# Performance work log

Measured on AMD Instinct MI355X. Metric: run time of the kernel, lower is better.

## Reference

```python
import jax, jax.numpy as jnp
import numpy as np

B = 65536
D_IN = 8
H1, H2 = 256, 256


def setup_inputs() -> dict:
    key = jax.random.key(0)
    ks = jax.random.split(key, 12)
    def lin(kw, kb, fan_in, fan_out):
        s = 1.0 / np.sqrt(fan_in)
        W = jax.random.uniform(kw, (fan_out, fan_in), jnp.float32, -s, s)
        b = jax.random.uniform(kb, (fan_out,), jnp.float32, -s, s)
        return W, b
    W0, b0 = lin(ks[0], ks[1], D_IN, H1)
    W1, b1 = lin(ks[2], ks[3], H1, H2)
    W2, b2 = lin(ks[4], ks[5], H2, 1)
    W3, b3 = lin(ks[6], ks[7], 1, 8)
    x_batch = jax.random.normal(ks[8], (B, D_IN), jnp.float32)
    scores_x_batch = jax.random.normal(ks[9], (B, D_IN), jnp.float32)
    c = jnp.zeros((), jnp.float32)  # init_val parameter
    return {"x_batch": x_batch, "scores_x_batch": scores_x_batch,
            "W0": W0, "b0": b0, "W1": W1, "b1": b1,
            "W2": W2, "b2": b2, "W3": W3, "b3": b3, "c": c}


def reference(x_batch, scores_x_batch, W0, b0, W1, b1, W2, b2, W3, b3, c):
    # singleforwardpass: tanh on all layers except the last
    def single(x):  # x: [8] -> [8]
        y = jnp.tanh(W0 @ x + b0)
        y = jnp.tanh(W1 @ y + b1)
        y = jnp.tanh(W2 @ y + b2)
        return W3 @ y + b3

    eye = jnp.eye(D_IN, dtype=x_batch.dtype)

    def per_sample(x, score):
        # jacobian(single, x).diag().sum() + dot(single(x), score) + c
        u, lin_fn = jax.linearize(single, x)
        J = jax.vmap(lin_fn)(eye)        # [8, 8] (columns of Jacobian as rows)
        div = jnp.trace(J)               # sum of Jacobian diagonal
        return c + div + jnp.dot(u, score)

    return jax.vmap(per_sample)(x_batch, scores_x_batch)  # [B]
```

## Files before the change

kernel.cpp:

```cpp
#include <hip/hip_runtime.h>
#include <hip/hip_bf16.h>

#define B_TOTAL 65536
#define H 256
#define TS 64
#define THREADS 512
#define STRIDE 264
#define KK 2.8853900817779268f

#define WS_W1   0
#define WS_W0B  65536
#define WS_AUX  67584
#define WS_XB   73728
#define WS_NEED_BYTES (147456 + 1048576)

typedef __attribute__((ext_vector_type(8))) short bf16x8;
typedef __attribute__((ext_vector_type(4))) float f32x4;

__device__ __forceinline__ float rsig(float kz) {
    float e = __builtin_amdgcn_exp2f(kz);
    return __builtin_amdgcn_rcpf(e + 1.0f);
}
__device__ __forceinline__ void tanh_r(float x, float& t, float& r) {
    r = rsig(KK * x);
    t = fmaf(-2.0f, r, 1.0f);
}
__device__ __forceinline__ float bf2f(ushort b) {
    union { unsigned u; float f; } v; v.u = ((unsigned)b) << 16;
    return v.f;
}
__device__ __forceinline__ ushort f2bf(float f) {
    union { float f; unsigned u; } v; v.f = f;
    unsigned r = v.u + 0x7fffu + ((v.u >> 16) & 1u);
    return (ushort)(r >> 16);
}
__device__ __forceinline__ ushort2 cvt2(float a, float b) {
    union { __hip_bfloat162 h; ushort2 u; } v;
    v.h = __float22bfloat162_rn(make_float2(a, b));
    return v.u;
}
__device__ __forceinline__ bf16x8 pack8(float4 a, float4 b) {
    union { bf16x8 v; ushort2 u[4]; } r;
    r.u[0] = cvt2(a.x, a.y); r.u[1] = cvt2(a.z, a.w);
    r.u[2] = cvt2(b.x, b.y); r.u[3] = cvt2(b.z, b.w);
    return r.v;
}

__global__ void prep(const float* __restrict__ W1, const float* __restrict__ W0,
                     const float* __restrict__ W3, const float* __restrict__ b0,
                     const float* __restrict__ b1, const float* __restrict__ W2,
                     const float* __restrict__ x, ushort* __restrict__ ws) {
    const int blk = blockIdx.x, tid = threadIdx.x;
    if (blk < 32) {
        int g = blk * 256 + tid;
        int jt = g >> 9;
        int ks = (g >> 6) & 7;
        int l  = g & 63;
        int row = jt * 16 + (l & 15);
        int k0  = ks * 32 + (l >> 4) * 8;
        ushort* dst = ws + WS_W1 + (size_t)g * 8;
        const float* src = W1 + (size_t)row * H + k0;
#pragma unroll
        for (int t = 0; t < 8; ++t) dst[t] = f2bf(src[t]);
    } else if (blk == 32) {
        const int j = tid;
        const float* wr = W0 + (size_t)j * 8;
        float4 wa = *(const float4*)wr, wb = *(const float4*)(wr + 4);
        float4 w3a = *(const float4*)W3, w3b = *(const float4*)(W3 + 4);
        float g0 = wa.x * w3a.x + wa.y * w3a.y + wa.z * w3a.z + wa.w * w3a.w
                 + wb.x * w3b.x + wb.y * w3b.y + wb.z * w3b.z + wb.w * w3b.w;
        float* aux = (float*)(ws + WS_AUX);
        aux[j]        = 4.f * g0;
        aux[256 + j]  = KK * b0[j];
        aux[512 + j]  = KK * b1[j];
        aux[768 + j]  = -2.f * W2[j];
        aux[1024 + j] = 4.f * W2[j];
        *(bf16x8*)(ws + WS_W0B + (size_t)j * 8) = pack8(wa, wb);
    } else {
        const int s = (blk - 33) * 256 + tid;
        const float* xr = x + (size_t)s * 8;
        *(bf16x8*)(ws + WS_XB + (size_t)s * 8) =
            pack8(*(const float4*)xr, *(const float4*)(xr + 4));
    }
}

template<int XB>
__launch_bounds__(THREADS, 4)
__global__ void fused_mlp(const float* __restrict__ x_batch,
                          const float* __restrict__ scores,
                          const float* __restrict__ b2,
                          const float* __restrict__ W3, const float* __restrict__ b3,
                          const float* __restrict__ cptr,
                          const ushort* __restrict__ ws,
                          float* __restrict__ out) {
    __shared__ ushort Y0[TS][STRIDE];
    __shared__ ushort DG[TS][STRIDE];
    __shared__ float  Z2p[8][TS];
    __shared__ float  Trp[8][TS];

    const int tid  = threadIdx.x;
    const int lane = tid & 63;
    const int w    = tid >> 6;
    const int bs   = blockIdx.x * TS;
    const int cl   = lane & 15;
    const int q    = lane >> 4;
    const int rq   = q * 4;
    const int j0   = w * 32;

    const ushort* pW  = ws + WS_W1 + (size_t)(2 * w) * 4096 + (size_t)lane * 8;
    const ushort* w0b = ws + WS_W0B;
    const float*  aux = (const float*)(ws + WS_AUX);
    const float*  G4  = aux;
    const float*  KB0 = aux + 256;
    const float*  KB1 = aux + 512;
    const float*  WN  = aux + 768;
    const float*  W4  = aux + 1024;
    const ushort* xb  = ws + WS_XB;

    f32x4 l0[2][4];
    {
        bf16x8 bx[4];
#pragma unroll
        for (int st = 0; st < 4; ++st) {
            bf16x8 p = (bf16x8){0, 0, 0, 0, 0, 0, 0, 0};
            if (q == 0) {
                if (XB) {
                    p = *(const bf16x8*)(xb + (size_t)(bs + st * 16 + cl) * 8);
                } else {
                    const float* xr = x_batch + (size_t)(bs + st * 16 + cl) * 8;
                    p = pack8(*(const float4*)xr, *(const float4*)(xr + 4));
                }
            }
            bx[st] = p;
        }
        bf16x8 af0 = *(const bf16x8*)(w0b + (size_t)(j0 + cl) * 8);
        bf16x8 af1 = *(const bf16x8*)(w0b + (size_t)(j0 + 16 + cl) * 8);
#pragma unroll
        for (int st = 0; st < 4; ++st) {
            f32x4 z = (f32x4){0.f, 0.f, 0.f, 0.f};
            l0[0][st] = __builtin_amdgcn_mfma_f32_16x16x32_bf16(af0, bx[st], z, 0, 0, 0);
            l0[1][st] = __builtin_amdgcn_mfma_f32_16x16x32_bf16(af1, bx[st], z, 0, 0, 0);
        }
    }

    {
        float4 kb0 = *(const float4*)(KB0 + j0 + rq);
        float4 kb1 = *(const float4*)(KB0 + j0 + 16 + rq);
        float4 g40 = *(const float4*)(G4 + j0 + rq);
        float4 g41 = *(const float4*)(G4 + j0 + 16 + rq);
#pragma unroll
        for (int st = 0; st < 4; ++st) {
            const int row = st * 16 + cl;
#pragma unroll
            for (int jt = 0; jt < 2; ++jt) {
                f32x4 z = l0[jt][st];
                float4 kb = jt ? kb1 : kb0;
                float4 g4 = jt ? g41 : g40;
                float r0 = rsig(fmaf(KK, z[0], kb.x));
                float r1 = rsig(fmaf(KK, z[1], kb.y));
                float r2 = rsig(fmaf(KK, z[2], kb.z));
                float r3 = rsig(fmaf(KK, z[3], kb.w));
                float t0 = fmaf(-2.f, r0, 1.f), t1 = fmaf(-2.f, r1, 1.f);
                float t2 = fmaf(-2.f, r2, 1.f), t3 = fmaf(-2.f, r3, 1.f);
                ushort2 lo = cvt2(t0, t1), hi = cvt2(t2, t3);
                ushort4 vv; vv.x = lo.x; vv.y = lo.y; vv.z = hi.x; vv.w = hi.y;
                *(ushort4*)&Y0[row][j0 + jt * 16 + rq] = vv;
                float m0 = r0 * g4.x, m1 = r1 * g4.y, m2 = r2 * g4.z, m3 = r3 * g4.w;
                float d0 = fmaf(-m0, r0, m0), d1 = fmaf(-m1, r1, m1);
                float d2 = fmaf(-m2, r2, m2), d3 = fmaf(-m3, r3, m3);
                lo = cvt2(d0, d1); hi = cvt2(d2, d3);
                vv.x = lo.x; vv.y = lo.y; vv.z = hi.x; vv.w = hi.y;
                *(ushort4*)&DG[row][j0 + jt * 16 + rq] = vv;
            }
        }
    }
    __syncthreads();

    f32x4 facc[2][4], bacc[2][4];
#pragma unroll
    for (int jt = 0; jt < 2; ++jt)
#pragma unroll
        for (int st = 0; st < 4; ++st) {
            facc[jt][st] = (f32x4){0.f, 0.f, 0.f, 0.f};
            bacc[jt][st] = (f32x4){0.f, 0.f, 0.f, 0.f};
        }
#pragma unroll
    for (int ks = 0; ks < 8; ++ks) {
        const int k0 = ks * 32 + q * 8;
        bf16x8 wf0 = *(const bf16x8*)(pW + (size_t)ks * 512);
        bf16x8 wf1 = *(const bf16x8*)(pW + 4096 + (size_t)ks * 512);
#pragma unroll
        for (int st = 0; st < 4; ++st) {
            bf16x8 by = *(const bf16x8*)&Y0[st * 16 + cl][k0];
            bf16x8 bd = *(const bf16x8*)&DG[st * 16 + cl][k0];
            facc[0][st] = __builtin_amdgcn_mfma_f32_16x16x32_bf16(wf0, by, facc[0][st], 0, 0, 0);
            facc[1][st] = __builtin_amdgcn_mfma_f32_16x16x32_bf16(wf1, by, facc[1][st], 0, 0, 0);
            bacc[0][st] = __builtin_amdgcn_mfma_f32_16x16x32_bf16(wf0, bd, bacc[0][st], 0, 0, 0);
            bacc[1][st] = __builtin_amdgcn_mfma_f32_16x16x32_bf16(wf1, bd, bacc[1][st], 0, 0, 0);
        }
    }

    {
        float4 kb0 = *(const float4*)(KB1 + j0 + rq);
        float4 kb1 = *(const float4*)(KB1 + j0 + 16 + rq);
        float4 wn0 = *(const float4*)(WN + j0 + rq);
        float4 wn1 = *(const float4*)(WN + j0 + 16 + rq);
        float4 w40 = *(const float4*)(W4 + j0 + rq);
        float4 w41 = *(const float4*)(W4 + j0 + 16 + rq);
        float zp0 = 0.25f * ((w40.x + w40.y) + (w40.z + w40.w)
                           + (w41.x + w41.y) + (w41.z + w41.w));
#pragma unroll
        for (int st = 0; st < 4; ++st) {
            float zp = zp0, tp = 0.f;
#pragma unroll
            for (int jt = 0; jt < 2; ++jt) {
                f32x4 z  = facc[jt][st];
                f32x4 mm = bacc[jt][st];
                float4 kb = jt ? kb1 : kb0;
                float4 wn = jt ? wn1 : wn0;
                float4 w4 = jt ? w41 : w40;
                float r0 = rsig(fmaf(KK, z[0], kb.x));
                float r1 = rsig(fmaf(KK, z[1], kb.y));
                float r2 = rsig(fmaf(KK, z[2], kb.z));
                float r3 = rsig(fmaf(KK, z[3], kb.w));
                zp = fmaf(wn.x, r0, zp); zp = fmaf(wn.y, r1, zp);
                zp = fmaf(wn.z, r2, zp); zp = fmaf(wn.w, r3, zp);
                float m0 = r0 * w4.x, m1 = r1 * w4.y, m2 = r2 * w4.z, m3 = r3 * w4.w;
                float a0 = fmaf(-m0, r0, m0), a1 = fmaf(-m1, r1, m1);
                float a2 = fmaf(-m2, r2, m2), a3 = fmaf(-m3, r3, m3);
                tp = fmaf(a0, mm[0], tp); tp = fmaf(a1, mm[1], tp);
                tp = fmaf(a2, mm[2], tp); tp = fmaf(a3, mm[3], tp);
            }
            zp += __shfl_xor(zp, 16);
            zp += __shfl_xor(zp, 32);
            tp += __shfl_xor(tp, 16);
            tp += __shfl_xor(tp, 32);
            if (lane < 16) {
                Z2p[w][st * 16 + lane] = zp;
                Trp[w][st * 16 + lane] = tp;
            }
        }
    }
    __syncthreads();

    if (tid < TS) {
        const int s = tid;
        float z2 = b2[0], tr = 0.f;
#pragma unroll
        for (int k = 0; k < 8; ++k) { z2 += Z2p[k][s]; tr += Trp[k][s]; }
        float y2, r2;
        tanh_r(z2, y2, r2);
        float m2 = 4.0f * r2;
        float dy2 = fmaf(-m2, r2, m2);
        float4 w3a = *(const float4*)W3;
        float4 w3b = *(const float4*)(W3 + 4);
        float4 b3a = *(const float4*)b3;
        float4 b3b = *(const float4*)(b3 + 4);
        const float* sc = scores + (size_t)(bs + s) * 8;
        float4 s0 = *(const float4*)sc;
        float4 s1 = *(const float4*)(sc + 4);
        float p1 = w3a.x * s0.x + w3a.y * s0.y + w3a.z * s0.z + w3a.w * s0.w
                 + w3b.x * s1.x + w3b.y * s1.y + w3b.z * s1.z + w3b.w * s1.w;
        float p2 = b3a.x * s0.x + b3a.y * s0.y + b3a.z * s0.z + b3a.w * s0.w
                 + b3b.x * s1.x + b3b.y * s1.y + b3b.z * s1.z + b3b.w * s1.w;
        out[bs + s] = cptr[0] + dy2 * tr + fmaf(y2, p1, p2);
    }
}

extern "C" void kernel_launch(void* const* d_in, const int* in_sizes, int n_in,
                              void* d_out, int out_size, void* d_ws, size_t ws_size,
                              hipStream_t stream) {
    const float* x  = (const float*)d_in[0];
    const float* sc = (const float*)d_in[1];
    const float* W0 = (const float*)d_in[2];
    const float* b0 = (const float*)d_in[3];
    const float* W1 = (const float*)d_in[4];
    const float* b1 = (const float*)d_in[5];
    const float* W2 = (const float*)d_in[6];
    const float* b2 = (const float*)d_in[7];
    const float* W3 = (const float*)d_in[8];
    const float* b3 = (const float*)d_in[9];
    const float* c  = (const float*)d_in[10];
    float* out = (float*)d_out;
    ushort* ws = (ushort*)d_ws;

    const bool xb = ws_size >= (size_t)WS_NEED_BYTES;
    hipLaunchKernelGGL(prep, dim3(xb ? 289 : 33), dim3(256), 0, stream,
                       W1, W0, W3, b0, b1, W2, x, ws);
    if (xb) {
        hipLaunchKernelGGL(fused_mlp<1>, dim3(B_TOTAL / TS), dim3(THREADS), 0, stream,
                           x, sc, b2, W3, b3, c, ws, out);
    } else {
        hipLaunchKernelGGL(fused_mlp<0>, dim3(B_TOTAL / TS), dim3(THREADS), 0, stream,
                           x, sc, b2, W3, b3, c, ws, out);
    }
}
```

Measured before the change: 30.92 us.

## Process two sample tiles per block, hoisting constants and prefetching next tile's inputs

Each block now loops over two 64-sample tiles instead of one, halving the grid size. Per-neuron constants (biases, gains, layer-2 weights) are loaded once per block and reused across both tiles. The next tile's x inputs are prefetched during the current tile's layer-1 MFMA work. Costs are fewer blocks to spread across CUs (512 instead of 1024), an extra barrier per tile and higher register pressure.

```diff
diff --git a/kernel.cpp b/kernel.cpp
--- a/kernel.cpp
+++ b/kernel.cpp
@@ -4,6 +4,7 @@
 #define B_TOTAL 65536
 #define H 256
 #define TS 64
+#define NT 2
 #define THREADS 512
 #define STRIDE 264
 #define KK 2.8853900817779268f
@@ -95,13 +96,13 @@
                           float* __restrict__ out) {
     __shared__ ushort Y0[TS][STRIDE];
     __shared__ ushort DG[TS][STRIDE];
-    __shared__ float  Z2p[8][TS];
-    __shared__ float  Trp[8][TS];
+    __shared__ float  Z2p[8][NT][TS];
+    __shared__ float  Trp[8][NT][TS];
 
     const int tid  = threadIdx.x;
     const int lane = tid & 63;
     const int w    = tid >> 6;
-    const int bs   = blockIdx.x * TS;
+    const int bs0  = blockIdx.x * (TS * NT);
     const int cl   = lane & 15;
     const int q    = lane >> 4;
     const int rq   = q * 4;
@@ -117,44 +118,57 @@
     const float*  W4  = aux + 1024;
     const ushort* xb  = ws + WS_XB;
 
-    f32x4 l0[2][4];
-    {
-        bf16x8 bx[4];
-#pragma unroll
-        for (int st = 0; st < 4; ++st) {
-            bf16x8 p = (bf16x8){0, 0, 0, 0, 0, 0, 0, 0};
-            if (q == 0) {
-                if (XB) {
-                    p = *(const bf16x8*)(xb + (size_t)(bs + st * 16 + cl) * 8);
-                } else {
-                    const float* xr = x_batch + (size_t)(bs + st * 16 + cl) * 8;
-                    p = pack8(*(const float4*)xr, *(const float4*)(xr + 4));
-                }
-            }
-            bx[st] = p;
-        }
-        bf16x8 af0 = *(const bf16x8*)(w0b + (size_t)(j0 + cl) * 8);
-        bf16x8 af1 = *(const bf16x8*)(w0b + (size_t)(j0 + 16 + cl) * 8);
-#pragma unroll
-        for (int st = 0; st < 4; ++st) {
-            f32x4 z = (f32x4){0.f, 0.f, 0.f, 0.f};
-            l0[0][st] = __builtin_amdgcn_mfma_f32_16x16x32_bf16(af0, bx[st], z, 0, 0, 0);
-            l0[1][st] = __builtin_amdgcn_mfma_f32_16x16x32_bf16(af1, bx[st], z, 0, 0, 0);
-        }
-    }
-
-    {
-        float4 kb0 = *(const float4*)(KB0 + j0 + rq);
-        float4 kb1 = *(const float4*)(KB0 + j0 + 16 + rq);
-        float4 g40 = *(const float4*)(G4 + j0 + rq);
-        float4 g41 = *(const float4*)(G4 + j0 + 16 + rq);
+    float4 kb00 = *(const float4*)(KB0 + j0 + rq);
+    float4 kb01 = *(const float4*)(KB0 + j0 + 16 + rq);
+    float4 g40  = *(const float4*)(G4 + j0 + rq);
+    float4 g41  = *(const float4*)(G4 + j0 + 16 + rq);
+    float4 kb10 = *(const float4*)(KB1 + j0 + rq);
+    float4 kb11 = *(const float4*)(KB1 + j0 + 16 + rq);
+    float4 wn0  = *(const float4*)(WN + j0 + rq);
+    float4 wn1  = *(const float4*)(WN + j0 + 16 + rq);
+    float4 w40  = *(const float4*)(W4 + j0 + rq);
+    float4 w41  = *(const float4*)(W4 + j0 + 16 + rq);
+    float zp0 = 0.25f * ((w40.x + w40.y) + (w40.z + w40.w)
+                       + (w41.x + w41.y) + (w41.z + w41.w));
+
+    bf16x8 bx[4];
+#pragma unroll
+    for (int st = 0; st < 4; ++st) {
+        bf16x8 p = (bf16x8){0, 0, 0, 0, 0, 0, 0, 0};
+        if (q == 0) {
+            if (XB) {
+                p = *(const bf16x8*)(xb + (size_t)(bs0 + st * 16 + cl) * 8);
+            } else {
+                const float* xr = x_batch + (size_t)(bs0 + st * 16 + cl) * 8;
+                p = pack8(*(const float4*)xr, *(const float4*)(xr + 4));
+            }
+        }
+        bx[st] = p;
+    }
+
+#pragma unroll
+    for (int t = 0; t < NT; ++t) {
+        const int bs = bs0 + t * TS;
+
+        f32x4 l0[2][4];
+        {
+            bf16x8 af0 = *(const bf16x8*)(w0b + (size_t)(j0 + cl) * 8);
+            bf16x8 af1 = *(const bf16x8*)(w0b + (size_t)(j0 + 16 + cl) * 8);
+#pragma unroll
+            for (int st = 0; st < 4; ++st) {
+                f32x4 z = (f32x4){0.f, 0.f, 0.f, 0.f};
+                l0[0][st] = __builtin_amdgcn_mfma_f32_16x16x32_bf16(af0, bx[st], z, 0, 0, 0);
+                l0[1][st] = __builtin_amdgcn_mfma_f32_16x16x32_bf16(af1, bx[st], z, 0, 0, 0);
+            }
+        }
+
 #pragma unroll
         for (int st = 0; st < 4; ++st) {
             const int row = st * 16 + cl;
 #pragma unroll
             for (int jt = 0; jt < 2; ++jt) {
                 f32x4 z = l0[jt][st];
-                float4 kb = jt ? kb1 : kb0;
+                float4 kb = jt ? kb01 : kb00;
                 float4 g4 = jt ? g41 : g40;
                 float r0 = rsig(fmaf(KK, z[0], kb.x));
                 float r1 = rsig(fmaf(KK, z[1], kb.y));
@@ -173,42 +187,48 @@
                 *(ushort4*)&DG[row][j0 + jt * 16 + rq] = vv;
             }
         }
-    }
-    __syncthreads();
-
-    f32x4 facc[2][4], bacc[2][4];
-#pragma unroll
-    for (int jt = 0; jt < 2; ++jt)
-#pragma unroll
-        for (int st = 0; st < 4; ++st) {
-            facc[jt][st] = (f32x4){0.f, 0.f, 0.f, 0.f};
-            bacc[jt][st] = (f32x4){0.f, 0.f, 0.f, 0.f};
-        }
-#pragma unroll
-    for (int ks = 0; ks < 8; ++ks) {
-        const int k0 = ks * 32 + q * 8;
-        bf16x8 wf0 = *(const bf16x8*)(pW + (size_t)ks * 512);
-        bf16x8 wf1 = *(const bf16x8*)(pW + 4096 + (size_t)ks * 512);
-#pragma unroll
-        for (int st = 0; st < 4; ++st) {
-            bf16x8 by = *(const bf16x8*)&Y0[st * 16 + cl][k0];
-            bf16x8 bd = *(const bf16x8*)&DG[st * 16 + cl][k0];
-            facc[0][st] = __builtin_amdgcn_mfma_f32_16x16x32_bf16(wf0, by, facc[0][st], 0, 0, 0);
-            facc[1][st] = __builtin_amdgcn_mfma_f32_16x16x32_bf16(wf1, by, facc[1][st], 0, 0, 0);
-            bacc[0][st] = __builtin_amdgcn_mfma_f32_16x16x32_bf16(wf0, bd, bacc[0][st], 0, 0, 0);
-            bacc[1][st] = __builtin_amdgcn_mfma_f32_16x16x32_bf16(wf1, bd, bacc[1][st], 0, 0, 0);
-        }
-    }
-
-    {
-        float4 kb0 = *(const float4*)(KB1 + j0 + rq);
-        float4 kb1 = *(const float4*)(KB1 + j0 + 16 + rq);
-        float4 wn0 = *(const float4*)(WN + j0 + rq);
-        float4 wn1 = *(const float4*)(WN + j0 + 16 + rq);
-        float4 w40 = *(const float4*)(W4 + j0 + rq);
-        float4 w41 = *(const float4*)(W4 + j0 + 16 + rq);
-        float zp0 = 0.25f * ((w40.x + w40.y) + (w40.z + w40.w)
-                           + (w41.x + w41.y) + (w41.z + w41.w));
+        __syncthreads();
+
+        f32x4 facc[2][4], bacc[2][4];
+#pragma unroll
+        for (int jt = 0; jt < 2; ++jt)
+#pragma unroll
+            for (int st = 0; st < 4; ++st) {
+                facc[jt][st] = (f32x4){0.f, 0.f, 0.f, 0.f};
+                bacc[jt][st] = (f32x4){0.f, 0.f, 0.f, 0.f};
+            }
+#pragma unroll
+        for (int ks = 0; ks < 8; ++ks) {
+            const int k0 = ks * 32 + q * 8;
+            bf16x8 wf0 = *(const bf16x8*)(pW + (size_t)ks * 512);
+            bf16x8 wf1 = *(const bf16x8*)(pW + 4096 + (size_t)ks * 512);
+#pragma unroll
+            for (int st = 0; st < 4; ++st) {
+                bf16x8 by = *(const bf16x8*)&Y0[st * 16 + cl][k0];
+                bf16x8 bd = *(const bf16x8*)&DG[st * 16 + cl][k0];
+                facc[0][st] = __builtin_amdgcn_mfma_f32_16x16x32_bf16(wf0, by, facc[0][st], 0, 0, 0);
+                facc[1][st] = __builtin_amdgcn_mfma_f32_16x16x32_bf16(wf1, by, facc[1][st], 0, 0, 0);
+                bacc[0][st] = __builtin_amdgcn_mfma_f32_16x16x32_bf16(wf0, bd, bacc[0][st], 0, 0, 0);
+                bacc[1][st] = __builtin_amdgcn_mfma_f32_16x16x32_bf16(wf1, bd, bacc[1][st], 0, 0, 0);
+            }
+        }
+
+        if (t + 1 < NT) {
+#pragma unroll
+            for (int st = 0; st < 4; ++st) {
+                bf16x8 p = (bf16x8){0, 0, 0, 0, 0, 0, 0, 0};
+                if (q == 0) {
+                    if (XB) {
+                        p = *(const bf16x8*)(xb + (size_t)(bs0 + TS + st * 16 + cl) * 8);
+                    } else {
+                        const float* xr = x_batch + (size_t)(bs0 + TS + st * 16 + cl) * 8;
+                        p = pack8(*(const float4*)xr, *(const float4*)(xr + 4));
+                    }
+                }
+                bx[st] = p;
+            }
+        }
+
 #pragma unroll
         for (int st = 0; st < 4; ++st) {
             float zp = zp0, tp = 0.f;
@@ -216,7 +236,7 @@
             for (int jt = 0; jt < 2; ++jt) {
                 f32x4 z  = facc[jt][st];
                 f32x4 mm = bacc[jt][st];
-                float4 kb = jt ? kb1 : kb0;
+                float4 kb = jt ? kb11 : kb10;
                 float4 wn = jt ? wn1 : wn0;
                 float4 w4 = jt ? w41 : w40;
                 float r0 = rsig(fmaf(KK, z[0], kb.x));
@@ -236,18 +256,18 @@
             tp += __shfl_xor(tp, 16);
             tp += __shfl_xor(tp, 32);
             if (lane < 16) {
-                Z2p[w][st * 16 + lane] = zp;
-                Trp[w][st * 16 + lane] = tp;
-            }
-        }
-    }
-    __syncthreads();
-
-    if (tid < TS) {
-        const int s = tid;
+                Z2p[w][t][st * 16 + lane] = zp;
+                Trp[w][t][st * 16 + lane] = tp;
+            }
+        }
+        __syncthreads();
+    }
+
+    if (tid < TS * NT) {
+        const int tt = tid >> 6, i = tid & 63;
         float z2 = b2[0], tr = 0.f;
 #pragma unroll
-        for (int k = 0; k < 8; ++k) { z2 += Z2p[k][s]; tr += Trp[k][s]; }
+        for (int k = 0; k < 8; ++k) { z2 += Z2p[k][tt][i]; tr += Trp[k][tt][i]; }
         float y2, r2;
         tanh_r(z2, y2, r2);
         float m2 = 4.0f * r2;
@@ -256,14 +276,14 @@
         float4 w3b = *(const float4*)(W3 + 4);
         float4 b3a = *(const float4*)b3;
         float4 b3b = *(const float4*)(b3 + 4);
-        const float* sc = scores + (size_t)(bs + s) * 8;
+        const float* sc = scores + (size_t)(bs0 + tid) * 8;
         float4 s0 = *(const float4*)sc;
         float4 s1 = *(const float4*)(sc + 4);
         float p1 = w3a.x * s0.x + w3a.y * s0.y + w3a.z * s0.z + w3a.w * s0.w
                  + w3b.x * s1.x + w3b.y * s1.y + w3b.z * s1.z + w3b.w * s1.w;
         float p2 = b3a.x * s0.x + b3a.y * s0.y + b3a.z * s0.z + b3a.w * s0.w
                  + b3b.x * s1.x + b3b.y * s1.y + b3b.z * s1.z + b3b.w * s1.w;
-        out[bs + s] = cptr[0] + dy2 * tr + fmaf(y2, p1, p2);
+        out[bs0 + tid] = cptr[0] + dy2 * tr + fmaf(y2, p1, p2);
     }
 }
 
@@ -288,10 +308,10 @@
     hipLaunchKernelGGL(prep, dim3(xb ? 289 : 33), dim3(256), 0, stream,
                        W1, W0, W3, b0, b1, W2, x, ws);
     if (xb) {
-        hipLaunchKernelGGL(fused_mlp<1>, dim3(B_TOTAL / TS), dim3(THREADS), 0, stream,
+        hipLaunchKernelGGL(fused_mlp<1>, dim3(B_TOTAL / (TS * NT)), dim3(THREADS), 0, stream,
                            x, sc, b2, W3, b3, c, ws, out);
     } else {
-        hipLaunchKernelGGL(fused_mlp<0>, dim3(B_TOTAL / TS), dim3(THREADS), 0, stream,
+        hipLaunchKernelGGL(fused_mlp<0>, dim3(B_TOTAL / (TS * NT)), dim3(THREADS), 0, stream,
                            x, sc, b2, W3, b3, c, ws, out);
     }
 }
```

Result: slower. 50.13 us (+62.1%).
